# Optimization experiments

Hardware: AMD Instinct MI355X
Metric: run time of the kernel (lower is better)

## Reference

```python
import jax, jax.numpy as jnp
import numpy as np

INPUT_SIZE = 1024
HIDDEN_SIZE = 1024
BATCH = 32768
LEARNING_RATE = 0.01
# First call: time_stamps is empty -> temporal_weight = 1.0
TEMPORAL_WEIGHT = 1.0


def setup_inputs() -> dict:
    key = jax.random.key(0)
    kx, kw = jax.random.split(key)
    x = jax.random.normal(kx, (BATCH, INPUT_SIZE), dtype=jnp.float32)
    # nn.Parameter(torch.randn(input_size, hidden_size) * 0.1)
    W = jax.random.normal(kw, (INPUT_SIZE, HIDDEN_SIZE), dtype=jnp.float32) * 0.1
    return {"x": x, "W": W}


def reference(x, W):
    # Forward: hidden = tanh(x @ W)
    hidden = jnp.tanh(x @ W)  # [B, H]
    # Hebbian update: sum_b lr * outer(x_b, hidden_b) * w(t) / B == lr * w(t)/B * x^T @ hidden
    batch = x.shape[0]
    delta_w = (LEARNING_RATE * TEMPORAL_WEIGHT / batch) * (x.T @ hidden)  # [I, H]
    new_W = jnp.clip(W + delta_w, -1.0, 1.0)
    return hidden, new_W
```

## Files before the change

kernel.cpp:

```cpp
#include <hip/hip_runtime.h>
#include <cstdint>

#define BB 32768
#define II 1024
#define HH 1024
#define SPLIT 16
#define KCH (BB/SPLIT)
#define NT1 (II/64)
#define NT2 (KCH/64)

typedef _Float16 f16;
typedef _Float16 f16x4 __attribute__((ext_vector_type(4)));
typedef _Float16 f16x8 __attribute__((ext_vector_type(8)));
typedef float f32x4 __attribute__((ext_vector_type(4)));

typedef const __attribute__((address_space(1))) void gvoid_t;
typedef __attribute__((address_space(3))) void lvoid_t;

__device__ __forceinline__ void gload16(const void* g, void* l){
    __builtin_amdgcn_global_load_lds((gvoid_t*)g, (lvoid_t*)l, 16, 0, 0);
}

__device__ __forceinline__ float tanh_fast(float s){
    float a = fabsf(s);
    float e = __expf(-2.0f * a);
    float t = __fdividef(1.0f - e, 1.0f + e);
    return s < 0.0f ? -t : t;
}

__global__ __launch_bounds__(256) void k_prep(const float* __restrict__ in,
                                              f16* __restrict__ cvt_out,
                                              f16* __restrict__ tr_out,
                                              int C, int R){
    __shared__ float lt[64*67];
    const int t = threadIdx.x;
    const int r0 = blockIdx.x*64, c0 = blockIdx.y*64;
    #pragma unroll
    for (int p=0; p<4; ++p){
        int r = p*16 + (t>>4);
        int c = (t&15)*4;
        float4 v = *(const float4*)&in[(size_t)(r0+r)*C + c0 + c];
        if (cvt_out){
            f16x4 hv = {(f16)v.x,(f16)v.y,(f16)v.z,(f16)v.w};
            *(f16x4*)&cvt_out[(size_t)(r0+r)*C + c0 + c] = hv;
        }
        lt[r*67 + c+0] = v.x;
        lt[r*67 + c+1] = v.y;
        lt[r*67 + c+2] = v.z;
        lt[r*67 + c+3] = v.w;
    }
    __syncthreads();
    const int c = t>>2, rb = (t&3)*16;
    f16x8 a, b;
    #pragma unroll
    for (int e=0; e<8; ++e) a[e] = (f16)lt[(rb+e)*67 + c];
    #pragma unroll
    for (int e=0; e<8; ++e) b[e] = (f16)lt[(rb+8+e)*67 + c];
    f16* o = &tr_out[(size_t)(c0+c)*R + r0 + rb];
    *(f16x8*)o = a;
    *(f16x8*)(o+8) = b;
}

template<bool MT>
__device__ __forceinline__ void stage_half(const f16* __restrict__ panel, int ld,
                                           int row0, int kcol0, char* lds_half,
                                           int wid, int lane){
    #pragma unroll
    for (int r=0;r<2;++r){
        int o = r*8192 + wid*1024 + lane*16;
        int rr = o>>7;
        int c0 = (o&127) ^ ((rr&7)<<4);
        if constexpr (!MT){
            const f16* src = panel + (size_t)(row0 + rr)*ld + kcol0 + (c0>>1);
            gload16(src, lds_half + r*8192 + wid*1024);
        } else {
            int h    = row0 + rr;
            int babs = kcol0 + (c0>>1);
            const f16* src = panel + (((size_t)(h>>4)*(BB>>4) + (babs>>4))<<8)
                                   + ((h&15)<<4) + (babs&8);
            gload16(src, lds_half + r*8192 + wid*1024);
        }
    }
}

#define RD_A(BUFA, mh) { \
    _Pragma("unroll") for (int m_=0;m_<4;++m_){ \
        af[m_][0] = *(const f16x8*)((BUFA) + rowA + (mh)*8192 + m_*2048 + ksw0); \
        af[m_][1] = *(const f16x8*)((BUFA) + rowA + (mh)*8192 + m_*2048 + ksw1); }}

#define RD_B(BUFB, nh) { \
    _Pragma("unroll") for (int n_=0;n_<2;++n_){ \
        bf[(nh)*2+n_][0] = *(const f16x8*)((BUFB) + rowB + (nh)*4096 + n_*2048 + ksw0); \
        bf[(nh)*2+n_][1] = *(const f16x8*)((BUFB) + rowB + (nh)*4096 + n_*2048 + ksw1); }}

#define MFMA_Q(mh,nh) { \
    __builtin_amdgcn_s_setprio(1); \
    _Pragma("unroll") for (int m_=0;m_<4;++m_){ \
      _Pragma("unroll") for (int n_=0;n_<2;++n_){ \
        _Pragma("unroll") for (int ks_=0;ks_<2;++ks_){ \
          acc[(mh)*4+m_][(nh)*2+n_] = __builtin_amdgcn_mfma_f32_16x16x32_f16( \
              af[m_][ks_], bf[(nh)*2+n_][ks_], acc[(mh)*4+m_][(nh)*2+n_], 0,0,0); }}} \
    __builtin_amdgcn_s_setprio(0); }

#define PH_SYNC1 { __builtin_amdgcn_s_barrier(); \
    asm volatile("s_waitcnt lgkmcnt(0)" ::: "memory"); \
    __builtin_amdgcn_sched_barrier(0); }
#define PH_SYNC2 { __builtin_amdgcn_s_barrier(); }

template<bool BMT>
__device__ __forceinline__ void kloop8(const f16* __restrict__ Ap, int lda, int arow0,
                                       const f16* __restrict__ Bp, int ldb, int brow0,
                                       int kbase, int nt, char* sm,
                                       f32x4 (&acc)[8][4])
{
    const int t = threadIdx.x, lane = t & 63, wid = t >> 6;
    const int wr = wid >> 2, wc = wid & 3;
    const int fr = lane & 15, kg = lane >> 4;
    const int mask = nt - 1;
    char* const A0 = sm;
    char* const B0 = sm + 32768;
    char* const A1 = sm + 65536;
    char* const B1 = sm + 98304;
    const int rowA = wr*16384 + fr*128;
    const int rowB = (wc>>1)*16384 + (wc&1)*8192 + fr*128;
    const int ksw0 = ((kg    ) ^ (fr & 7)) << 4;
    const int ksw1 = ((kg + 4) ^ (fr & 7)) << 4;

    f16x8 af[4][2], bf[4][2];

    stage_half<false>(Ap, lda, arow0 +   0, kbase +  0, A0,         wid, lane);
    stage_half<false>(Ap, lda, arow0 + 128, kbase +  0, A0 + 16384, wid, lane);
    stage_half<BMT  >(Bp, ldb, brow0 +   0, kbase +  0, B0,         wid, lane);
    stage_half<BMT  >(Bp, ldb, brow0 + 128, kbase +  0, B0 + 16384, wid, lane);
    stage_half<BMT  >(Bp, ldb, brow0 +   0, kbase + 64, B1,         wid, lane);
    stage_half<false>(Ap, lda, arow0 +   0, kbase + 64, A1,         wid, lane);
    asm volatile("s_waitcnt vmcnt(4)" ::: "memory");
    __builtin_amdgcn_s_barrier();

    const int ni = nt >> 1;
    for (int it = 0; it < ni; ++it){
        const int k1 = (2*it + 1) * 64;
        const int k2 = ((2*it + 2) & mask) * 64;
        const int k3 = ((2*it + 3) & mask) * 64;
        RD_A(A0, 0); RD_B(B0, 0);
        stage_half<false>(Ap, lda, arow0 + 128, kbase + k1, A1 + 16384, wid, lane);
        PH_SYNC1; MFMA_Q(0,0); PH_SYNC2;
        RD_B(B0, 1);
        stage_half<BMT>(Bp, ldb, brow0 + 128, kbase + k1, B1 + 16384, wid, lane);
        PH_SYNC1; MFMA_Q(0,1); PH_SYNC2;
        RD_A(A0, 1);
        stage_half<BMT>(Bp, ldb, brow0 +   0, kbase + k2, B0, wid, lane);
        PH_SYNC1; MFMA_Q(1,0); PH_SYNC2;
        stage_half<false>(Ap, lda, arow0 +   0, kbase + k2, A0, wid, lane);
        PH_SYNC1; MFMA_Q(1,1);
        asm volatile("s_waitcnt vmcnt(4)" ::: "memory");
        __builtin_amdgcn_s_barrier();
        RD_A(A1, 0); RD_B(B1, 0);
        stage_half<false>(Ap, lda, arow0 + 128, kbase + k2, A0 + 16384, wid, lane);
        PH_SYNC1; MFMA_Q(0,0); PH_SYNC2;
        RD_B(B1, 1);
        stage_half<BMT>(Bp, ldb, brow0 + 128, kbase + k2, B0 + 16384, wid, lane);
        PH_SYNC1; MFMA_Q(0,1); PH_SYNC2;
        RD_A(A1, 1);
        stage_half<BMT>(Bp, ldb, brow0 +   0, kbase + k3, B1, wid, lane);
        PH_SYNC1; MFMA_Q(1,0); PH_SYNC2;
        stage_half<false>(Ap, lda, arow0 +   0, kbase + k3, A1, wid, lane);
        PH_SYNC1; MFMA_Q(1,1);
        asm volatile("s_waitcnt vmcnt(4)" ::: "memory");
        __builtin_amdgcn_s_barrier();
    }
    asm volatile("s_waitcnt vmcnt(0)" ::: "memory");
    __builtin_amdgcn_s_barrier();
}

__global__ __launch_bounds__(512,2) void k_gemm1(const f16* __restrict__ xf,
                                                 const f16* __restrict__ wt,
                                                 float* __restrict__ hidden,
                                                 f16* __restrict__ ht){
    __shared__ char sm[131072];
    const int bid = (int)blockIdx.x;
    const int swz = (bid & 7)*64 + (bid >> 3);
    const int btile = swz >> 2, htile = swz & 3;
    f32x4 acc[8][4] = {};
    kloop8<false>(xf, II, btile*256, wt, II, htile*256, 0, NT1, sm, acc);

    const int t = threadIdx.x, lane = t & 63, wid = t >> 6;
    const int wr = wid >> 2, wc = wid & 3;
    const int fr = lane & 15, kg = lane >> 4;
    const int b_base = btile*256 + wr*128 + kg*4;
    const int h_base = htile*256 + wc*64 + fr;
    #pragma unroll
    for (int mf=0; mf<8; ++mf){
        const int b = b_base + mf*16;
        #pragma unroll
        for (int nf=0; nf<4; ++nf){
            const int h = h_base + nf*16;
            float t0 = tanh_fast(acc[mf][nf][0]);
            float t1 = tanh_fast(acc[mf][nf][1]);
            float t2 = tanh_fast(acc[mf][nf][2]);
            float t3 = tanh_fast(acc[mf][nf][3]);
            f16x4 hv = {(f16)t0,(f16)t1,(f16)t2,(f16)t3};
            *(f16x4*)&ht[(((size_t)(h>>4)*(BB>>4) + (b>>4))<<8) + ((h&15)<<4) + (b&15)] = hv;
            hidden[(size_t)(b+0)*HH + h] = t0;
            hidden[(size_t)(b+1)*HH + h] = t1;
            hidden[(size_t)(b+2)*HH + h] = t2;
            hidden[(size_t)(b+3)*HH + h] = t3;
        }
    }
}

__global__ __launch_bounds__(512,2) void k_gemm2(const f16* __restrict__ xt,
                                                 const f16* __restrict__ ht,
                                                 f16* __restrict__ part){
    __shared__ char sm[131072];
    const int bid = (int)blockIdx.x;
    const int swz = (bid & 7)*32 + (bid >> 3);
    const int split = swz >> 4, tile = swz & 15;
    const int itile = tile & 3, htile = tile >> 2;
    f32x4 acc[8][4] = {};
    kloop8<true>(xt, BB, itile*256, ht, BB, htile*256, split*KCH, NT2, sm, acc);

    const int t = threadIdx.x, lane = t & 63, wid = t >> 6;
    const int wr = wid >> 2, wc = wid & 3;
    const int fr = lane & 15, kg = lane >> 4;
    const size_t pb = (size_t)split*II*HH;
    #pragma unroll
    for (int mf=0; mf<8; ++mf){
        const int i0 = itile*256 + wr*128 + mf*16 + kg*4;
        #pragma unroll
        for (int nf=0; nf<4; ++nf){
            const int h = htile*256 + wc*64 + nf*16 + fr;
            f16x4 pv = {(f16)acc[mf][nf][0],(f16)acc[mf][nf][1],
                        (f16)acc[mf][nf][2],(f16)acc[mf][nf][3]};
            *(f16x4*)&part[pb + (((size_t)(i0>>4)*(HH>>4) + (h>>4))<<8) + ((h&15)<<4) + (i0&15)] = pv;
        }
    }
}

__global__ __launch_bounds__(256) void k_final(const f16* __restrict__ part,
                                               const float* __restrict__ W,
                                               float* __restrict__ outW){
    const int T = (int)blockIdx.x*256 + threadIdx.x;
    const int mt = T >> 5;
    const int hl = (T & 31) >> 1;
    const int ihalf = T & 1;
    const int i0 = (mt >> 6)*16 + ihalf*8;
    const int h  = (mt & 63)*16 + hl;
    const size_t po = ((size_t)mt << 8) + (hl << 4) + ihalf*8;
    float s[8] = {};
    #pragma unroll
    for (int sp=0; sp<SPLIT; ++sp){
        f16x8 p = *(const f16x8*)&part[(size_t)sp*1048576 + po];
        #pragma unroll
        for (int e=0;e<8;++e) s[e] += (float)p[e];
    }
    const float SCALE = 3.0517578125e-07f;
    #pragma unroll
    for (int e=0;e<8;++e){
        const size_t o = (size_t)(i0+e)*HH + h;
        outW[o] = fminf(1.f, fmaxf(-1.f, fmaf(SCALE, s[e], W[o])));
    }
}

extern "C" void kernel_launch(void* const* d_in, const int* in_sizes, int n_in,
                              void* d_out, int out_size, void* d_ws, size_t ws_size,
                              hipStream_t stream){
    (void)in_sizes; (void)n_in; (void)out_size; (void)ws_size;
    const float* x = (const float*)d_in[0];
    const float* W = (const float*)d_in[1];
    float* hidden = (float*)d_out;
    float* outW   = hidden + (size_t)BB*HH;
    char* ws = (char*)d_ws;
    f16* xf   = (f16*)(ws);
    f16* xt   = (f16*)(ws + 67108864ull);
    f16* ht   = (f16*)(ws + 134217728ull);
    f16* wt   = (f16*)(ws + 201326592ull);
    f16* part = (f16*)(ws);

    k_prep<<<dim3(BB/64, II/64), 256, 0, stream>>>(x, xf, xt, II, BB);
    k_prep<<<dim3(II/64, HH/64), 256, 0, stream>>>(W, nullptr, wt, HH, II);
    k_gemm1<<<dim3((BB/256)*(HH/256)), 512, 0, stream>>>(xf, wt, hidden, ht);
    k_gemm2<<<dim3(16*SPLIT), 512, 0, stream>>>(xt, ht, part);
    k_final<<<dim3((II*HH)/(256*8)), 256, 0, stream>>>(part, W, outW);
}
```

Before: 233.7 us.

## Shrink GEMM tiles to 128x128 with simple double-buffered loop and higher occupancy

Replaces the 256x256 tile, 8-phase interleaved K loop with a 128x128 tile and a simple double-buffered loop, halving LDS use and raising launch_bounds occupancy to 4 blocks per SIMD group. The second GEMM's split-K drops from 16 to 8 with 64 tiles per split. Smaller tiles lower arithmetic intensity and increase global/L2 traffic, and the fine-grained phase interleaving of loads and MFMAs is lost, in exchange for more blocks and simpler scheduling.

New measurement: 267.2 us. 1.14x slower.

```diff
diff --git a/kernel.cpp b/kernel.cpp
--- a/kernel.cpp
+++ b/kernel.cpp
@@ -4,7 +4,7 @@
 #define BB 32768
 #define II 1024
 #define HH 1024
-#define SPLIT 16
+#define SPLIT 8
 #define KCH (BB/SPLIT)
 #define NT1 (II/64)
 #define NT2 (KCH/64)
@@ -83,117 +83,87 @@
     }
 }
 
-#define RD_A(BUFA, mh) { \
-    _Pragma("unroll") for (int m_=0;m_<4;++m_){ \
-        af[m_][0] = *(const f16x8*)((BUFA) + rowA + (mh)*8192 + m_*2048 + ksw0); \
-        af[m_][1] = *(const f16x8*)((BUFA) + rowA + (mh)*8192 + m_*2048 + ksw1); }}
-
-#define RD_B(BUFB, nh) { \
-    _Pragma("unroll") for (int n_=0;n_<2;++n_){ \
-        bf[(nh)*2+n_][0] = *(const f16x8*)((BUFB) + rowB + (nh)*4096 + n_*2048 + ksw0); \
-        bf[(nh)*2+n_][1] = *(const f16x8*)((BUFB) + rowB + (nh)*4096 + n_*2048 + ksw1); }}
-
-#define MFMA_Q(mh,nh) { \
-    __builtin_amdgcn_s_setprio(1); \
-    _Pragma("unroll") for (int m_=0;m_<4;++m_){ \
-      _Pragma("unroll") for (int n_=0;n_<2;++n_){ \
-        _Pragma("unroll") for (int ks_=0;ks_<2;++ks_){ \
-          acc[(mh)*4+m_][(nh)*2+n_] = __builtin_amdgcn_mfma_f32_16x16x32_f16( \
-              af[m_][ks_], bf[(nh)*2+n_][ks_], acc[(mh)*4+m_][(nh)*2+n_], 0,0,0); }}} \
-    __builtin_amdgcn_s_setprio(0); }
-
-#define PH_SYNC1 { __builtin_amdgcn_s_barrier(); \
-    asm volatile("s_waitcnt lgkmcnt(0)" ::: "memory"); \
-    __builtin_amdgcn_sched_barrier(0); }
-#define PH_SYNC2 { __builtin_amdgcn_s_barrier(); }
-
 template<bool BMT>
-__device__ __forceinline__ void kloop8(const f16* __restrict__ Ap, int lda, int arow0,
+__device__ __forceinline__ void kloop2(const f16* __restrict__ Ap, int lda, int arow0,
                                        const f16* __restrict__ Bp, int ldb, int brow0,
                                        int kbase, int nt, char* sm,
-                                       f32x4 (&acc)[8][4])
+                                       f32x4 (&acc)[4][2])
 {
     const int t = threadIdx.x, lane = t & 63, wid = t >> 6;
     const int wr = wid >> 2, wc = wid & 3;
     const int fr = lane & 15, kg = lane >> 4;
-    const int mask = nt - 1;
     char* const A0 = sm;
-    char* const B0 = sm + 32768;
-    char* const A1 = sm + 65536;
-    char* const B1 = sm + 98304;
-    const int rowA = wr*16384 + fr*128;
-    const int rowB = (wc>>1)*16384 + (wc&1)*8192 + fr*128;
+    char* const B0 = sm + 16384;
+    char* const A1 = sm + 32768;
+    char* const B1 = sm + 49152;
+    const int rowA = wr*8192 + fr*128;
+    const int rowB = wc*4096 + fr*128;
     const int ksw0 = ((kg    ) ^ (fr & 7)) << 4;
     const int ksw1 = ((kg + 4) ^ (fr & 7)) << 4;
-
-    f16x8 af[4][2], bf[4][2];
-
-    stage_half<false>(Ap, lda, arow0 +   0, kbase +  0, A0,         wid, lane);
-    stage_half<false>(Ap, lda, arow0 + 128, kbase +  0, A0 + 16384, wid, lane);
-    stage_half<BMT  >(Bp, ldb, brow0 +   0, kbase +  0, B0,         wid, lane);
-    stage_half<BMT  >(Bp, ldb, brow0 + 128, kbase +  0, B0 + 16384, wid, lane);
-    stage_half<BMT  >(Bp, ldb, brow0 +   0, kbase + 64, B1,         wid, lane);
-    stage_half<false>(Ap, lda, arow0 +   0, kbase + 64, A1,         wid, lane);
-    asm volatile("s_waitcnt vmcnt(4)" ::: "memory");
-    __builtin_amdgcn_s_barrier();
-
-    const int ni = nt >> 1;
-    for (int it = 0; it < ni; ++it){
-        const int k1 = (2*it + 1) * 64;
-        const int k2 = ((2*it + 2) & mask) * 64;
-        const int k3 = ((2*it + 3) & mask) * 64;
-        RD_A(A0, 0); RD_B(B0, 0);
-        stage_half<false>(Ap, lda, arow0 + 128, kbase + k1, A1 + 16384, wid, lane);
-        PH_SYNC1; MFMA_Q(0,0); PH_SYNC2;
-        RD_B(B0, 1);
-        stage_half<BMT>(Bp, ldb, brow0 + 128, kbase + k1, B1 + 16384, wid, lane);
-        PH_SYNC1; MFMA_Q(0,1); PH_SYNC2;
-        RD_A(A0, 1);
-        stage_half<BMT>(Bp, ldb, brow0 +   0, kbase + k2, B0, wid, lane);
-        PH_SYNC1; MFMA_Q(1,0); PH_SYNC2;
-        stage_half<false>(Ap, lda, arow0 +   0, kbase + k2, A0, wid, lane);
-        PH_SYNC1; MFMA_Q(1,1);
-        asm volatile("s_waitcnt vmcnt(4)" ::: "memory");
+    f16x8 af[4][2], bf[2][2];
+
+    stage_half<false>(Ap, lda, arow0, kbase +  0, A0, wid, lane);
+    stage_half<BMT  >(Bp, ldb, brow0, kbase +  0, B0, wid, lane);
+    stage_half<false>(Ap, lda, arow0, kbase + 64, A1, wid, lane);
+    stage_half<BMT  >(Bp, ldb, brow0, kbase + 64, B1, wid, lane);
+
+    for (int tt = 0; tt < nt; ++tt){
+        if (tt < nt-1){ asm volatile("s_waitcnt vmcnt(4)" ::: "memory"); }
+        else          { asm volatile("s_waitcnt vmcnt(0)" ::: "memory"); }
         __builtin_amdgcn_s_barrier();
-        RD_A(A1, 0); RD_B(B1, 0);
-        stage_half<false>(Ap, lda, arow0 + 128, kbase + k2, A0 + 16384, wid, lane);
-        PH_SYNC1; MFMA_Q(0,0); PH_SYNC2;
-        RD_B(B1, 1);
-        stage_half<BMT>(Bp, ldb, brow0 + 128, kbase + k2, B0 + 16384, wid, lane);
-        PH_SYNC1; MFMA_Q(0,1); PH_SYNC2;
-        RD_A(A1, 1);
-        stage_half<BMT>(Bp, ldb, brow0 +   0, kbase + k3, B1, wid, lane);
-        PH_SYNC1; MFMA_Q(1,0); PH_SYNC2;
-        stage_half<false>(Ap, lda, arow0 +   0, kbase + k3, A1, wid, lane);
-        PH_SYNC1; MFMA_Q(1,1);
-        asm volatile("s_waitcnt vmcnt(4)" ::: "memory");
+        char* const A = (tt & 1) ? A1 : A0;
+        char* const B = (tt & 1) ? B1 : B0;
+        #pragma unroll
+        for (int m_=0;m_<4;++m_){
+            af[m_][0] = *(const f16x8*)(A + rowA + m_*2048 + ksw0);
+            af[m_][1] = *(const f16x8*)(A + rowA + m_*2048 + ksw1);
+        }
+        #pragma unroll
+        for (int n_=0;n_<2;++n_){
+            bf[n_][0] = *(const f16x8*)(B + rowB + n_*2048 + ksw0);
+            bf[n_][1] = *(const f16x8*)(B + rowB + n_*2048 + ksw1);
+        }
+        asm volatile("s_waitcnt lgkmcnt(0)" ::: "memory");
+        __builtin_amdgcn_sched_barrier(0);
         __builtin_amdgcn_s_barrier();
-    }
-    asm volatile("s_waitcnt vmcnt(0)" ::: "memory");
-    __builtin_amdgcn_s_barrier();
-}
-
-__global__ __launch_bounds__(512,2) void k_gemm1(const f16* __restrict__ xf,
+        if (tt + 2 < nt){
+            stage_half<false>(Ap, lda, arow0, kbase + (tt+2)*64, A, wid, lane);
+            stage_half<BMT  >(Bp, ldb, brow0, kbase + (tt+2)*64, B, wid, lane);
+        }
+        __builtin_amdgcn_s_setprio(1);
+        #pragma unroll
+        for (int m_=0;m_<4;++m_)
+            #pragma unroll
+            for (int n_=0;n_<2;++n_)
+                #pragma unroll
+                for (int ks_=0;ks_<2;++ks_)
+                    acc[m_][n_] = __builtin_amdgcn_mfma_f32_16x16x32_f16(
+                        af[m_][ks_], bf[n_][ks_], acc[m_][n_], 0, 0, 0);
+        __builtin_amdgcn_s_setprio(0);
+    }
+}
+
+__global__ __launch_bounds__(512,4) void k_gemm1(const f16* __restrict__ xf,
                                                  const f16* __restrict__ wt,
                                                  float* __restrict__ hidden,
                                                  f16* __restrict__ ht){
-    __shared__ char sm[131072];
+    __shared__ char sm[65536];
     const int bid = (int)blockIdx.x;
-    const int swz = (bid & 7)*64 + (bid >> 3);
-    const int btile = swz >> 2, htile = swz & 3;
-    f32x4 acc[8][4] = {};
-    kloop8<false>(xf, II, btile*256, wt, II, htile*256, 0, NT1, sm, acc);
+    const int swz = (bid & 7)*256 + (bid >> 3);
+    const int btile = swz >> 3, htile = swz & 7;
+    f32x4 acc[4][2] = {};
+    kloop2<false>(xf, II, btile*128, wt, II, htile*128, 0, NT1, sm, acc);
 
     const int t = threadIdx.x, lane = t & 63, wid = t >> 6;
     const int wr = wid >> 2, wc = wid & 3;
     const int fr = lane & 15, kg = lane >> 4;
-    const int b_base = btile*256 + wr*128 + kg*4;
-    const int h_base = htile*256 + wc*64 + fr;
-    #pragma unroll
-    for (int mf=0; mf<8; ++mf){
+    const int b_base = btile*128 + wr*64 + kg*4;
+    const int h_base = htile*128 + wc*32 + fr;
+    #pragma unroll
+    for (int mf=0; mf<4; ++mf){
         const int b = b_base + mf*16;
         #pragma unroll
-        for (int nf=0; nf<4; ++nf){
+        for (int nf=0; nf<2; ++nf){
             const int h = h_base + nf*16;
             float t0 = tanh_fast(acc[mf][nf][0]);
             float t1 = tanh_fast(acc[mf][nf][1]);
@@ -209,27 +179,27 @@
     }
 }
 
-__global__ __launch_bounds__(512,2) void k_gemm2(const f16* __restrict__ xt,
+__global__ __launch_bounds__(512,4) void k_gemm2(const f16* __restrict__ xt,
                                                  const f16* __restrict__ ht,
                                                  f16* __restrict__ part){
-    __shared__ char sm[131072];
+    __shared__ char sm[65536];
     const int bid = (int)blockIdx.x;
-    const int swz = (bid & 7)*32 + (bid >> 3);
-    const int split = swz >> 4, tile = swz & 15;
-    const int itile = tile & 3, htile = tile >> 2;
-    f32x4 acc[8][4] = {};
-    kloop8<true>(xt, BB, itile*256, ht, BB, htile*256, split*KCH, NT2, sm, acc);
+    const int swz = (bid & 7)*64 + (bid >> 3);
+    const int split = swz >> 6, tile = swz & 63;
+    const int itile = tile >> 3, htile = tile & 7;
+    f32x4 acc[4][2] = {};
+    kloop2<true>(xt, BB, itile*128, ht, BB, htile*128, split*KCH, NT2, sm, acc);
 
     const int t = threadIdx.x, lane = t & 63, wid = t >> 6;
     const int wr = wid >> 2, wc = wid & 3;
     const int fr = lane & 15, kg = lane >> 4;
     const size_t pb = (size_t)split*II*HH;
     #pragma unroll
-    for (int mf=0; mf<8; ++mf){
-        const int i0 = itile*256 + wr*128 + mf*16 + kg*4;
-        #pragma unroll
-        for (int nf=0; nf<4; ++nf){
-            const int h = htile*256 + wc*64 + nf*16 + fr;
+    for (int mf=0; mf<4; ++mf){
+        const int i0 = itile*128 + wr*64 + mf*16 + kg*4;
+        #pragma unroll
+        for (int nf=0; nf<2; ++nf){
+            const int h = htile*128 + wc*32 + nf*16 + fr;
             f16x4 pv = {(f16)acc[mf][nf][0],(f16)acc[mf][nf][1],
                         (f16)acc[mf][nf][2],(f16)acc[mf][nf][3]};
             *(f16x4*)&part[pb + (((size_t)(i0>>4)*(HH>>4) + (h>>4))<<8) + ((h&15)<<4) + (i0&15)] = pv;
@@ -279,7 +249,7 @@
 
     k_prep<<<dim3(BB/64, II/64), 256, 0, stream>>>(x, xf, xt, II, BB);
     k_prep<<<dim3(II/64, HH/64), 256, 0, stream>>>(W, nullptr, wt, HH, II);
-    k_gemm1<<<dim3((BB/256)*(HH/256)), 512, 0, stream>>>(xf, wt, hidden, ht);
-    k_gemm2<<<dim3(16*SPLIT), 512, 0, stream>>>(xt, ht, part);
+    k_gemm1<<<dim3((BB/128)*(HH/128)), 512, 0, stream>>>(xf, wt, hidden, ht);
+    k_gemm2<<<dim3(64*SPLIT), 512, 0, stream>>>(xt, ht, part);
     k_final<<<dim3((II*HH)/(256*8)), 256, 0, stream>>>(part, W, outW);
 }
```
